# Performance work log

Hardware: AMD Instinct MI355X
Metric: run time of the kernel (lower is better)

Reference implementation:

```python
import jax, jax.numpy as jnp
import numpy as np

B, IN_DIM, HID, OUT_DIM = 32768, 784, 256, 1000
L, CURV = 3, 1e-3
LOG2_H = 8  # log2(HID)
EPS_BN = 1e-5

def _layer_param_sizes():
    return [(HID // (2 * (1 << (l % LOG2_H)))) * 2 for l in range(L)]

def setup_inputs():
    key = jax.random.key(0)
    ks = jax.random.split(key, 4)
    total = sum(_layer_param_sizes())  # 448
    return {
        "x": jax.random.normal(ks[0], (B, IN_DIM), jnp.float32),
        "fc1_w": jax.random.normal(ks[1], (HID, IN_DIM), jnp.float32) / np.sqrt(IN_DIM).astype(np.float32),
        "fc1_b": jnp.zeros((HID,), jnp.float32),
        "bn1_gamma": jnp.ones((HID,), jnp.float32),
        "bn1_beta": jnp.zeros((HID,), jnp.float32),
        "bf_params": jax.random.normal(ks[2], (total,), jnp.float32) * 0.01,
        "bn2_gamma": jnp.ones((HID,), jnp.float32),
        "bn2_beta": jnp.zeros((HID,), jnp.float32),
        "fc2_w": jax.random.normal(ks[3], (OUT_DIM, HID), jnp.float32) / np.sqrt(HID).astype(np.float32),
        "fc2_b": jnp.zeros((OUT_DIM,), jnp.float32),
    }

def _batchnorm(h, gamma, beta):
    # training-mode BatchNorm1d: batch mean / biased variance
    mu = jnp.mean(h, axis=0)
    var = jnp.mean(jnp.square(h - mu), axis=0)
    return gamma * (h - mu) * jax.lax.rsqrt(var + EPS_BN) + beta

def _log_map0(x, c):
    # Poincare ball log map at origin: artanh(sqrt(c)|x|) * x / (sqrt(c)|x|)
    sn = jnp.sqrt(c) * jnp.linalg.norm(x, axis=-1, keepdims=True)
    sn = jnp.clip(sn, 1e-7, 1.0 - 1e-6)
    return (jnp.arctanh(sn) / sn) * x

def _exp_map0(u, c):
    sn = jnp.maximum(jnp.sqrt(c) * jnp.linalg.norm(u, axis=-1, keepdims=True), 1e-7)
    return (jnp.tanh(sn) / sn) * u

def _hyper_butterfly(h, params, c):
    u = _log_map0(h, c)
    off = 0
    for l in range(L):
        bs = 1 << (l % LOG2_H)      # half-block size at stage l
        nb = HID // (2 * bs)        # number of 2x2-rotation blocks
        p = params[off:off + 2 * nb]
        a = p[:nb][None, :, None]   # [1, nb, 1]
        b = p[nb:][None, :, None]
        v = u.reshape(-1, nb, 2, bs)
        x1, x2 = v[:, :, 0], v[:, :, 1]
        y1 = a * x1 + b * x2
        y2 = -b * x1 + a * x2
        u = jnp.stack([y1, y2], axis=2).reshape(-1, HID)
        off += 2 * nb
    return _exp_map0(u, c)

def reference(x, fc1_w, fc1_b, bn1_gamma, bn1_beta, bf_params, bn2_gamma, bn2_beta, fc2_w, fc2_b):
    h = x @ fc1_w.T + fc1_b
    h = jax.nn.relu(_batchnorm(h, bn1_gamma, bn1_beta))
    ht = _hyper_butterfly(h, bf_params, CURV)
    ht = jax.nn.relu(_batchnorm(ht, bn2_gamma, bn2_beta))
    return ht @ fc2_w.T + fc2_b
```

## Files before the change

### kernel.cpp

```cpp
#include <hip/hip_runtime.h>
#include <math.h>

#define NBATCH 32768
#define IND    784
#define KPAD1  800
#define HIDD   256
#define OUTD   1000
#define OUTDP  1024

typedef _Float16 half8  __attribute__((ext_vector_type(8)));
typedef _Float16 half4v __attribute__((ext_vector_type(4)));
typedef float    floatx4 __attribute__((ext_vector_type(4)));

#define GAS __attribute__((address_space(1)))
#define LAS __attribute__((address_space(3)))

__device__ __forceinline__ void gld16(const void* g, void* l) {
    __builtin_amdgcn_global_load_lds((const GAS void*)g, (LAS void*)l, 16, 0, 0);
}

__device__ __forceinline__ float wave_allreduce_sum(float v) {
    #pragma unroll
    for (int off = 32; off >= 1; off >>= 1) v += __shfl_xor(v, off);
    return v;
}

__global__ __launch_bounds__(256)
void prep_kernel(const float* __restrict__ w1, _Float16* __restrict__ w1h,
                 const float* __restrict__ w2, _Float16* __restrict__ w2h,
                 float* __restrict__ stat)
{
    const int tid = threadIdx.x;
    if (blockIdx.x == 0) {
        for (int j = tid; j < 1024 + 16; j += 256) stat[j] = 0.0f;
    }
    const int NW1 = HIDD * (KPAD1 / 8);
    const int NW2 = OUTDP * (HIDD / 8);
    for (int i = blockIdx.x * 256 + tid; i < NW1 + NW2; i += (int)gridDim.x * 256) {
        half8 o;
        if (i < NW1) {
            const int r = i / (KPAD1 / 8), c8 = (i % (KPAD1 / 8)) * 8;
            if (c8 + 8 <= IND) {
                const float* s = &w1[(size_t)r * IND + c8];
                float4 v0 = *(const float4*)s, v1 = *(const float4*)(s + 4);
                o[0]=(_Float16)v0.x; o[1]=(_Float16)v0.y; o[2]=(_Float16)v0.z; o[3]=(_Float16)v0.w;
                o[4]=(_Float16)v1.x; o[5]=(_Float16)v1.y; o[6]=(_Float16)v1.z; o[7]=(_Float16)v1.w;
            } else {
                #pragma unroll
                for (int j = 0; j < 8; ++j) o[j] = (_Float16)0.0f;
            }
            *(half8*)&w1h[(size_t)r * KPAD1 + c8] = o;
        } else {
            const int k = i - NW1;
            const int r = k >> 5, c8 = (k & 31) * 8;
            if (r < OUTD) {
                const float* s = &w2[(size_t)r * HIDD + c8];
                float4 v0 = *(const float4*)s, v1 = *(const float4*)(s + 4);
                o[0]=(_Float16)v0.x; o[1]=(_Float16)v0.y; o[2]=(_Float16)v0.z; o[3]=(_Float16)v0.w;
                o[4]=(_Float16)v1.x; o[5]=(_Float16)v1.y; o[6]=(_Float16)v1.z; o[7]=(_Float16)v1.w;
            } else {
                #pragma unroll
                for (int j = 0; j < 8; ++j) o[j] = (_Float16)0.0f;
            }
            *(half8*)&w2h[(size_t)r * HIDD + c8] = o;
        }
    }
}

__global__ __launch_bounds__(256, 2)
void gemm1_kernel(const float* __restrict__ x, const _Float16* __restrict__ w1h,
                  const float* __restrict__ b1, const float* __restrict__ zbuf,
                  float* __restrict__ h, float* __restrict__ sum1, float* __restrict__ ssq1)
{
    __shared__ __align__(16) float    ldsA[2][4096];
    __shared__ __align__(16) _Float16 ldsB[2][4096];
    __shared__ float redS[2][128], redQ[2][128];

    const int tid  = threadIdx.x;
    const int bid0 = blockIdx.x;
    const int vbid = (bid0 & 7) * 64 + (bid0 >> 3);
    const int bm = vbid >> 1, bn = vbid & 1;
    const int m0 = bm * 128, n0 = bn * 128;
    const int lane = tid & 63, wv = tid >> 6;
    const int wr = wv >> 1, wc = wv & 1;
    const int l15 = lane & 15, lg = lane >> 4;
    const int e7 = l15 & 7, e3 = l15 & 3;

    const int arow = lane >> 3, agp = (lane & 7) ^ arow;
    const int brow = lane >> 2, bgp = (lane & 3) ^ (brow & 3);
    const float*    Ab = x   + (size_t)(m0 + arow) * IND   + agp * 4;
    const _Float16* Bb = w1h + (size_t)(n0 + brow) * KPAD1 + bgp * 8;

    floatx4 acc[4][4];
    #pragma unroll
    for (int i = 0; i < 4; ++i)
        #pragma unroll
        for (int j = 0; j < 4; ++j) acc[i][j] = (floatx4){0.f, 0.f, 0.f, 0.f};

    auto STAGE = [&](int buf, int t) {
        const int t32 = t * 32;
        const bool aok = (t32 + agp * 4) < IND;
        #pragma unroll
        for (int c = 0; c < 4; ++c) {
            const int ch = wv + c * 4;
            const float* s = aok ? (Ab + (size_t)ch * 8 * IND + t32) : zbuf;
            gld16(s, &ldsA[buf][ch * 256]);
        }
        #pragma unroll
        for (int c = 0; c < 2; ++c) {
            const int ch = wv + c * 4;
            gld16(Bb + (size_t)ch * 16 * KPAD1 + t32, &ldsB[buf][ch * 512]);
        }
    };

    STAGE(0, 0);
    __syncthreads();

    int buf = 0;
    const int nt = KPAD1 / 32;
    for (int t = 0; t < nt; ++t) {
        if (t + 1 < nt) STAGE(buf ^ 1, t + 1);
        half8 af[4], bfr[4];
        #pragma unroll
        for (int i = 0; i < 4; ++i) {
            const int rc = wr * 8 + i * 2 + (l15 >> 3);
            const float* base = &ldsA[buf][rc * 256 + e7 * 32];
            float4 va = *(const float4*)(base + (((2 * lg)     ^ e7) * 4));
            float4 vb = *(const float4*)(base + (((2 * lg + 1) ^ e7) * 4));
            half8 hv;
            hv[0]=(_Float16)va.x; hv[1]=(_Float16)va.y; hv[2]=(_Float16)va.z; hv[3]=(_Float16)va.w;
            hv[4]=(_Float16)vb.x; hv[5]=(_Float16)vb.y; hv[6]=(_Float16)vb.z; hv[7]=(_Float16)vb.w;
            af[i] = hv;
        }
        #pragma unroll
        for (int j = 0; j < 4; ++j)
            bfr[j] = *(const half8*)&ldsB[buf][(wc * 4 + j) * 512 + l15 * 32 + ((lg ^ e3) * 8)];
        #pragma unroll
        for (int i = 0; i < 4; ++i)
            #pragma unroll
            for (int j = 0; j < 4; ++j)
                acc[i][j] = __builtin_amdgcn_mfma_f32_16x16x32_f16(bfr[j], af[i], acc[i][j], 0, 0, 0);
        __syncthreads();
        buf ^= 1;
    }

    float sJ[4][4], qJ[4][4];
    #pragma unroll
    for (int j = 0; j < 4; ++j)
        #pragma unroll
        for (int r = 0; r < 4; ++r) { sJ[j][r] = 0.f; qJ[j][r] = 0.f; }
    #pragma unroll
    for (int i = 0; i < 4; ++i) {
        const int m = m0 + wr * 64 + i * 16 + l15;
        #pragma unroll
        for (int j = 0; j < 4; ++j) {
            const int nb = n0 + wc * 64 + j * 16 + lg * 4;
            float4 bt = *reinterpret_cast<const float4*>(&b1[nb]);
            float v[4] = {acc[i][j][0] + bt.x, acc[i][j][1] + bt.y,
                          acc[i][j][2] + bt.z, acc[i][j][3] + bt.w};
            *reinterpret_cast<float4*>(&h[(size_t)m * HIDD + nb]) =
                make_float4(v[0], v[1], v[2], v[3]);
            #pragma unroll
            for (int r = 0; r < 4; ++r) { sJ[j][r] += v[r]; qJ[j][r] += v[r] * v[r]; }
        }
    }
    #pragma unroll
    for (int j = 0; j < 4; ++j)
        #pragma unroll
        for (int r = 0; r < 4; ++r) {
            float s = sJ[j][r], q = qJ[j][r];
            s += __shfl_xor(s, 1); s += __shfl_xor(s, 2);
            s += __shfl_xor(s, 4); s += __shfl_xor(s, 8);
            q += __shfl_xor(q, 1); q += __shfl_xor(q, 2);
            q += __shfl_xor(q, 4); q += __shfl_xor(q, 8);
            if (l15 == 0) {
                redS[wr][wc * 64 + j * 16 + lg * 4 + r] = s;
                redQ[wr][wc * 64 + j * 16 + lg * 4 + r] = q;
            }
        }
    __syncthreads();
    if (tid < 128) {
        atomicAdd(&sum1[n0 + tid], redS[0][tid] + redS[1][tid]);
        atomicAdd(&ssq1[n0 + tid], redQ[0][tid] + redQ[1][tid]);
    }
}

__global__ __launch_bounds__(256)
void mid_kernel(const float* __restrict__ h, const float* __restrict__ bfp,
                const float* __restrict__ sum1, const float* __restrict__ ssq1,
                const float* __restrict__ g1, const float* __restrict__ be1,
                _Float16* __restrict__ ht16, float* __restrict__ sum2, float* __restrict__ ssq2)
{
    __shared__ float s1sh[256], t1sh[256];
    __shared__ float bsum[4][256], bssq[4][256];
    const int tid  = threadIdx.x;
    {
        const float inv = 1.0f / (float)NBATCH;
        const float mu  = sum1[tid] * inv;
        const float var = fmaxf(ssq1[tid] * inv - mu * mu, 0.0f);
        const float rs  = 1.0f / sqrtf(var + 1e-5f);
        const float sj  = g1[tid] * rs;
        s1sh[tid] = sj;
        t1sh[tid] = fmaf(-mu, sj, be1[tid]);
    }
    __syncthreads();

    const int w    = tid >> 6;
    const int lane = tid & 63;
    const int row0 = blockIdx.x * 64 + w * 16;
    const int c0   = lane * 4;

    const float4 s1v = *reinterpret_cast<const float4*>(&s1sh[c0]);
    const float4 t1v = *reinterpret_cast<const float4*>(&t1sh[c0]);
    const float a0 = bfp[2 * lane],       a1 = bfp[2 * lane + 1];
    const float b0 = bfp[128 + 2 * lane], b1 = bfp[128 + 2 * lane + 1];
    const float a2 = bfp[256 + lane],     b2 = bfp[320 + lane];
    const float a3 = bfp[384 + (lane >> 1)], b3 = bfp[416 + (lane >> 1)];
    const float sgn = (lane & 1) ? -1.0f : 1.0f;
    const float sc  = sqrtf(1e-3f);

    float ps0 = 0, ps1 = 0, ps2 = 0, ps3 = 0;
    float q0 = 0, q1 = 0, q2 = 0, q3 = 0;

    for (int r = 0; r < 16; ++r) {
        const int row = row0 + r;
        const float4 v = *reinterpret_cast<const float4*>(&h[(size_t)row * HIDD + c0]);
        float x0 = fmaxf(fmaf(v.x, s1v.x, t1v.x), 0.0f);
        float x1 = fmaxf(fmaf(v.y, s1v.y, t1v.y), 0.0f);
        float x2 = fmaxf(fmaf(v.z, s1v.z, t1v.z), 0.0f);
        float x3 = fmaxf(fmaf(v.w, s1v.w, t1v.w), 0.0f);
        float n2 = x0 * x0 + x1 * x1 + x2 * x2 + x3 * x3;
        n2 = wave_allreduce_sum(n2);
        float sn = sc * sqrtf(n2);
        sn = fminf(fmaxf(sn, 1e-7f), 1.0f - 1e-6f);
        const float ls = atanhf(sn) / sn;
        x0 *= ls; x1 *= ls; x2 *= ls; x3 *= ls;
        const float y0 = fmaf(a0, x0,  b0 * x1);
        const float y1 = fmaf(a0, x1, -b0 * x0);
        const float y2 = fmaf(a1, x2,  b1 * x3);
        const float y3 = fmaf(a1, x3, -b1 * x2);
        const float z0 = fmaf(a2, y0,  b2 * y2);
        const float z1 = fmaf(a2, y1,  b2 * y3);
        const float z2 = fmaf(a2, y2, -b2 * y0);
        const float z3 = fmaf(a2, y3, -b2 * y1);
        const float p0 = __shfl_xor(z0, 1);
        const float p1 = __shfl_xor(z1, 1);
        const float p2 = __shfl_xor(z2, 1);
        const float p3 = __shfl_xor(z3, 1);
        const float w0 = fmaf(a3, z0, sgn * (b3 * p0));
        const float w1 = fmaf(a3, z1, sgn * (b3 * p1));
        const float w2 = fmaf(a3, z2, sgn * (b3 * p2));
        const float w3 = fmaf(a3, z3, sgn * (b3 * p3));
        float m2 = w0 * w0 + w1 * w1 + w2 * w2 + w3 * w3;
        m2 = wave_allreduce_sum(m2);
        const float sn2 = fmaxf(sc * sqrtf(m2), 1e-7f);
        const float es = tanhf(sn2) / sn2;
        const float o0 = es * w0, o1 = es * w1, o2 = es * w2, o3 = es * w3;
        half4v hv;
        hv[0] = (_Float16)(o0 * 65536.0f); hv[1] = (_Float16)(o1 * 65536.0f);
        hv[2] = (_Float16)(o2 * 65536.0f); hv[3] = (_Float16)(o3 * 65536.0f);
        *reinterpret_cast<half4v*>(&ht16[(size_t)row * HIDD + c0]) = hv;
        ps0 += o0; ps1 += o1; ps2 += o2; ps3 += o3;
        q0 += o0 * o0; q1 += o1 * o1; q2 += o2 * o2; q3 += o3 * o3;
    }

    bsum[w][c0 + 0] = ps0; bsum[w][c0 + 1] = ps1; bsum[w][c0 + 2] = ps2; bsum[w][c0 + 3] = ps3;
    bssq[w][c0 + 0] = q0;  bssq[w][c0 + 1] = q1;  bssq[w][c0 + 2] = q2;  bssq[w][c0 + 3] = q3;
    __syncthreads();
    if (tid < 256) {
        const float s = bsum[0][tid] + bsum[1][tid] + bsum[2][tid] + bsum[3][tid];
        const float q = bssq[0][tid] + bssq[1][tid] + bssq[2][tid] + bssq[3][tid];
        atomicAdd(&sum2[tid], s);
        atomicAdd(&ssq2[tid], q);
    }
}

__global__ __launch_bounds__(256, 3)
void gemm2_kernel(const _Float16* __restrict__ ht16, const _Float16* __restrict__ w2h,
                  const float* __restrict__ b2,
                  const float* __restrict__ sum2, const float* __restrict__ ssq2,
                  const float* __restrict__ g2, const float* __restrict__ be2,
                  float* __restrict__ out)
{
    __shared__ __align__(16) _Float16 ldsA[2][4096];
    __shared__ __align__(16) _Float16 ldsB[2][4096];
    __shared__ float sf[256], tf[256];

    const int tid = threadIdx.x;
    {
        const float inv = 1.0f / (float)NBATCH;
        const float mu  = sum2[tid] * inv;
        const float var = fmaxf(ssq2[tid] * inv - mu * mu, 0.0f);
        const float rs  = 1.0f / sqrtf(var + 1e-5f);
        const float sj  = g2[tid] * rs;
        sf[tid] = sj * (1024.0f / 65536.0f);
        tf[tid] = fmaf(-mu, sj, be2[tid]) * 1024.0f;
    }

    const int bid0 = blockIdx.x;
    const int vbid = (bid0 & 7) * 256 + (bid0 >> 3);
    const int bm = vbid >> 3, bn = vbid & 7;
    const int m0 = bm * 128, n0 = bn * 128;
    const int lane = tid & 63, wv = tid >> 6;
    const int wr = wv >> 1, wc = wv & 1;
    const int l15 = lane & 15, lg = lane >> 4;
    const int e3 = l15 & 3;

    const int srow = lane >> 2, sgp = (lane & 3) ^ (srow & 3);
    const _Float16* Ab = ht16 + (size_t)(m0 + srow) * HIDD + sgp * 8;
    const _Float16* Bb = w2h  + (size_t)(n0 + srow) * HIDD + sgp * 8;

    floatx4 acc[4][4];
    #pragma unroll
    for (int i = 0; i < 4; ++i)
        #pragma unroll
        for (int j = 0; j < 4; ++j) acc[i][j] = (floatx4){0.f, 0.f, 0.f, 0.f};

    auto STAGE = [&](int buf, int t) {
        const int t32 = t * 32;
        #pragma unroll
        for (int c = 0; c < 2; ++c) {
            const int ch = wv + c * 4;
            gld16(Ab + (size_t)ch * 16 * HIDD + t32, &ldsA[buf][ch * 512]);
            gld16(Bb + (size_t)ch * 16 * HIDD + t32, &ldsB[buf][ch * 512]);
        }
    };

    STAGE(0, 0);
    __syncthreads();

    int buf = 0;
    const int nt = HIDD / 32;
    for (int t = 0; t < nt; ++t) {
        if (t + 1 < nt) STAGE(buf ^ 1, t + 1);
        const int kb = t * 32 + lg * 8;
        float4 s0 = *(const float4*)&sf[kb], s1 = *(const float4*)&sf[kb + 4];
        float4 t0 = *(const float4*)&tf[kb], t1 = *(const float4*)&tf[kb + 4];
        half8 af[4], bfr[4];
        #pragma unroll
        for (int i = 0; i < 4; ++i) {
            half8 v = *(const half8*)&ldsA[buf][(wr * 4 + i) * 512 + l15 * 32 + ((lg ^ e3) * 8)];
            half8 hv;
            hv[0] = (_Float16)fmaxf(fmaf((float)v[0], s0.x, t0.x), 0.0f);
            hv[1] = (_Float16)fmaxf(fmaf((float)v[1], s0.y, t0.y), 0.0f);
            hv[2] = (_Float16)fmaxf(fmaf((float)v[2], s0.z, t0.z), 0.0f);
            hv[3] = (_Float16)fmaxf(fmaf((float)v[3], s0.w, t0.w), 0.0f);
            hv[4] = (_Float16)fmaxf(fmaf((float)v[4], s1.x, t1.x), 0.0f);
            hv[5] = (_Float16)fmaxf(fmaf((float)v[5], s1.y, t1.y), 0.0f);
            hv[6] = (_Float16)fmaxf(fmaf((float)v[6], s1.z, t1.z), 0.0f);
            hv[7] = (_Float16)fmaxf(fmaf((float)v[7], s1.w, t1.w), 0.0f);
            af[i] = hv;
        }
        #pragma unroll
        for (int j = 0; j < 4; ++j)
            bfr[j] = *(const half8*)&ldsB[buf][(wc * 4 + j) * 512 + l15 * 32 + ((lg ^ e3) * 8)];
        #pragma unroll
        for (int i = 0; i < 4; ++i)
            #pragma unroll
            for (int j = 0; j < 4; ++j)
                acc[i][j] = __builtin_amdgcn_mfma_f32_16x16x32_f16(bfr[j], af[i], acc[i][j], 0, 0, 0);
        __syncthreads();
        buf ^= 1;
    }

    const float invScale = 1.0f / 1024.0f;
    #pragma unroll
    for (int i = 0; i < 4; ++i) {
        const int m = m0 + wr * 64 + i * 16 + l15;
        #pragma unroll
        for (int j = 0; j < 4; ++j) {
            const int nb = n0 + wc * 64 + j * 16 + lg * 4;
            float bj[4];
            if (nb + 4 <= OUTD) {
                float4 bt = *reinterpret_cast<const float4*>(&b2[nb]);
                bj[0] = bt.x; bj[1] = bt.y; bj[2] = bt.z; bj[3] = bt.w;
            } else {
                #pragma unroll
                for (int r = 0; r < 4; ++r) bj[r] = (nb + r < OUTD) ? b2[nb + r] : 0.0f;
            }
            float v[4];
            #pragma unroll
            for (int r = 0; r < 4; ++r) v[r] = fmaf(acc[i][j][r], invScale, bj[r]);
            if (nb + 4 <= OUTD) {
                *reinterpret_cast<float4*>(&out[(size_t)m * OUTD + nb]) =
                    make_float4(v[0], v[1], v[2], v[3]);
            } else {
                #pragma unroll
                for (int r = 0; r < 4; ++r)
                    if (nb + r < OUTD) out[(size_t)m * OUTD + nb + r] = v[r];
            }
        }
    }
}

extern "C" void kernel_launch(void* const* d_in, const int* in_sizes, int n_in,
                              void* d_out, int out_size, void* d_ws, size_t ws_size,
                              hipStream_t stream)
{
    const float* x   = (const float*)d_in[0];
    const float* w1  = (const float*)d_in[1];
    const float* b1  = (const float*)d_in[2];
    const float* g1  = (const float*)d_in[3];
    const float* be1 = (const float*)d_in[4];
    const float* bfp = (const float*)d_in[5];
    const float* g2  = (const float*)d_in[6];
    const float* be2 = (const float*)d_in[7];
    const float* w2  = (const float*)d_in[8];
    const float* b2  = (const float*)d_in[9];

    float* out = (float*)d_out;
    char*  wsb = (char*)d_ws;

    _Float16* ht16 = (_Float16*)(wsb);
    _Float16* w1h  = (_Float16*)(wsb + 16777216);
    _Float16* w2h  = (_Float16*)(wsb + 17186816);
    float*    stat = (float*)  (wsb + 17711104);
    float* sum1 = stat;
    float* ssq1 = stat + 256;
    float* sum2 = stat + 512;
    float* ssq2 = stat + 768;
    float* zbuf = stat + 1024;

    float* h = out;

    prep_kernel<<<232, 256, 0, stream>>>(w1, w1h, w2, w2h, stat);
    gemm1_kernel<<<512, 256, 0, stream>>>(x, w1h, b1, zbuf, h, sum1, ssq1);
    mid_kernel<<<512, 256, 0, stream>>>(h, bfp, sum1, ssq1, g1, be1, ht16, sum2, ssq2);
    gemm2_kernel<<<2048, 256, 0, stream>>>(ht16, w2h, b2, sum2, ssq2, g2, be2, out);
}
```

Baseline: 133.1 us.

## Triple-buffer both GEMM main loops with prefetch distance two and vmcnt waits

Both GEMM kernels now keep three LDS stages instead of two and issue the global-to-LDS loads two k-tiles ahead. Each iteration ends with an explicit s_waitcnt on vmcnt plus a barrier instead of __syncthreads, so the newest tile's loads can stay in flight across the barrier. The loads for tiles past the end are redirected to the zero buffer, which keeps the loop uniform. This should hide more global-memory latency, mainly in the bandwidth-heavy first GEMM. The cost is more LDS per block, which may limit occupancy, plus hand-counted vmcnt values that must match the number of loads issued per stage.

Result: faster. 129.4 us (-2.8%).

```diff
diff --git a/kernel.cpp b/kernel.cpp
--- a/kernel.cpp
+++ b/kernel.cpp
@@ -14,6 +14,11 @@
 
 #define GAS __attribute__((address_space(1)))
 #define LAS __attribute__((address_space(3)))
+
+#define WAITVM_BAR(N)                                                      \
+    asm volatile("s_waitcnt vmcnt(" #N ") lgkmcnt(0)" ::: "memory");       \
+    __builtin_amdgcn_s_barrier();                                          \
+    __builtin_amdgcn_sched_barrier(0)
 
 __device__ __forceinline__ void gld16(const void* g, void* l) {
     __builtin_amdgcn_global_load_lds((const GAS void*)g, (LAS void*)l, 16, 0, 0);
@@ -72,8 +77,8 @@
                   const float* __restrict__ b1, const float* __restrict__ zbuf,
                   float* __restrict__ h, float* __restrict__ sum1, float* __restrict__ ssq1)
 {
-    __shared__ __align__(16) float    ldsA[2][4096];
-    __shared__ __align__(16) _Float16 ldsB[2][4096];
+    __shared__ __align__(16) float    ldsA[3][4096];
+    __shared__ __align__(16) _Float16 ldsB[3][4096];
     __shared__ float redS[2][128], redQ[2][128];
 
     const int tid  = threadIdx.x;
@@ -85,6 +90,7 @@
     const int wr = wv >> 1, wc = wv & 1;
     const int l15 = lane & 15, lg = lane >> 4;
     const int e7 = l15 & 7, e3 = l15 & 3;
+    const int nt = KPAD1 / 32;
 
     const int arow = lane >> 3, agp = (lane & 7) ^ arow;
     const int brow = lane >> 2, bgp = (lane & 3) ^ (brow & 3);
@@ -99,7 +105,8 @@
 
     auto STAGE = [&](int buf, int t) {
         const int t32 = t * 32;
-        const bool aok = (t32 + agp * 4) < IND;
+        const bool tok = t < nt;
+        const bool aok = tok && (t32 + agp * 4) < IND;
         #pragma unroll
         for (int c = 0; c < 4; ++c) {
             const int ch = wv + c * 4;
@@ -109,17 +116,20 @@
         #pragma unroll
         for (int c = 0; c < 2; ++c) {
             const int ch = wv + c * 4;
-            gld16(Bb + (size_t)ch * 16 * KPAD1 + t32, &ldsB[buf][ch * 512]);
+            const void* s = tok ? (const void*)(Bb + (size_t)ch * 16 * KPAD1 + t32)
+                                : (const void*)zbuf;
+            gld16(s, &ldsB[buf][ch * 512]);
         }
     };
 
     STAGE(0, 0);
-    __syncthreads();
+    STAGE(1, 1);
+    WAITVM_BAR(6);
 
     int buf = 0;
-    const int nt = KPAD1 / 32;
     for (int t = 0; t < nt; ++t) {
-        if (t + 1 < nt) STAGE(buf ^ 1, t + 1);
+        int nbuf = buf + 2; if (nbuf >= 3) nbuf -= 3;
+        STAGE(nbuf, t + 2);
         half8 af[4], bfr[4];
         #pragma unroll
         for (int i = 0; i < 4; ++i) {
@@ -140,8 +150,8 @@
             #pragma unroll
             for (int j = 0; j < 4; ++j)
                 acc[i][j] = __builtin_amdgcn_mfma_f32_16x16x32_f16(bfr[j], af[i], acc[i][j], 0, 0, 0);
-        __syncthreads();
-        buf ^= 1;
+        WAITVM_BAR(6);
+        buf = (buf + 1 == 3) ? 0 : buf + 1;
     }
 
     float sJ[4][4], qJ[4][4];
@@ -280,10 +290,10 @@
                   const float* __restrict__ b2,
                   const float* __restrict__ sum2, const float* __restrict__ ssq2,
                   const float* __restrict__ g2, const float* __restrict__ be2,
-                  float* __restrict__ out)
+                  const float* __restrict__ zbuf, float* __restrict__ out)
 {
-    __shared__ __align__(16) _Float16 ldsA[2][4096];
-    __shared__ __align__(16) _Float16 ldsB[2][4096];
+    __shared__ __align__(16) _Float16 ldsA[3][4096];
+    __shared__ __align__(16) _Float16 ldsB[3][4096];
     __shared__ float sf[256], tf[256];
 
     const int tid = threadIdx.x;
@@ -305,6 +315,7 @@
     const int wr = wv >> 1, wc = wv & 1;
     const int l15 = lane & 15, lg = lane >> 4;
     const int e3 = l15 & 3;
+    const int nt = HIDD / 32;
 
     const int srow = lane >> 2, sgp = (lane & 3) ^ (srow & 3);
     const _Float16* Ab = ht16 + (size_t)(m0 + srow) * HIDD + sgp * 8;
@@ -318,21 +329,27 @@
 
     auto STAGE = [&](int buf, int t) {
         const int t32 = t * 32;
+        const bool tok = t < nt;
         #pragma unroll
         for (int c = 0; c < 2; ++c) {
             const int ch = wv + c * 4;
-            gld16(Ab + (size_t)ch * 16 * HIDD + t32, &ldsA[buf][ch * 512]);
-            gld16(Bb + (size_t)ch * 16 * HIDD + t32, &ldsB[buf][ch * 512]);
+            const void* sa = tok ? (const void*)(Ab + (size_t)ch * 16 * HIDD + t32)
+                                 : (const void*)zbuf;
+            const void* sb = tok ? (const void*)(Bb + (size_t)ch * 16 * HIDD + t32)
+                                 : (const void*)zbuf;
+            gld16(sa, &ldsA[buf][ch * 512]);
+            gld16(sb, &ldsB[buf][ch * 512]);
         }
     };
 
     STAGE(0, 0);
-    __syncthreads();
+    STAGE(1, 1);
+    WAITVM_BAR(4);
 
     int buf = 0;
-    const int nt = HIDD / 32;
     for (int t = 0; t < nt; ++t) {
-        if (t + 1 < nt) STAGE(buf ^ 1, t + 1);
+        int nbuf = buf + 2; if (nbuf >= 3) nbuf -= 3;
+        STAGE(nbuf, t + 2);
         const int kb = t * 32 + lg * 8;
         float4 s0 = *(const float4*)&sf[kb], s1 = *(const float4*)&sf[kb + 4];
         float4 t0 = *(const float4*)&tf[kb], t1 = *(const float4*)&tf[kb + 4];
@@ -359,9 +376,10 @@
             #pragma unroll
             for (int j = 0; j < 4; ++j)
                 acc[i][j] = __builtin_amdgcn_mfma_f32_16x16x32_f16(bfr[j], af[i], acc[i][j], 0, 0, 0);
-        __syncthreads();
-        buf ^= 1;
-    }
+        WAITVM_BAR(4);
+        buf = (buf + 1 == 3) ? 0 : buf + 1;
+    }
+    asm volatile("s_waitcnt vmcnt(0)" ::: "memory");
 
     const float invScale = 1.0f / 1024.0f;
     #pragma unroll
@@ -426,5 +444,5 @@
     prep_kernel<<<232, 256, 0, stream>>>(w1, w1h, w2, w2h, stat);
     gemm1_kernel<<<512, 256, 0, stream>>>(x, w1h, b1, zbuf, h, sum1, ssq1);
     mid_kernel<<<512, 256, 0, stream>>>(h, bfp, sum1, ssq1, g1, be1, ht16, sum2, ssq2);
-    gemm2_kernel<<<2048, 256, 0, stream>>>(ht16, w2h, b2, sum2, ssq2, g2, be2, out);
-}
+    gemm2_kernel<<<2048, 256, 0, stream>>>(ht16, w2h, b2, sum2, ssq2, g2, be2, zbuf, out);
+}
```
